# Kernel tuning notes

Measured on AMD Instinct MI355X. Metric: run time of the kernel, lower is better.

The kernel has to match this reference:

```python
import jax, jax.numpy as jnp
import numpy as np

DIM = 256
HEADS = 8
DHEAD = 32          # dim // 8
WIN = 128           # attn_window
NBLOCKS = 4
FF_INNER = int(DIM * 4 * 2 / 3)  # 682
SCALE = DHEAD ** -0.5


def layernorm(x, g, b):
    mu = jnp.mean(x, axis=-1, keepdims=True)
    var = jnp.mean((x - mu) ** 2, axis=-1, keepdims=True)
    return (x - mu) * jax.lax.rsqrt(var + 1e-5) * g + b


def look_around(x):
    # x: (b, h, nw, w, d) -> (b, h, nw, 3w, d); prev/current/next window, zero-padded ends
    nw = x.shape[2]
    p = jnp.pad(x, ((0, 0), (0, 0), (1, 1), (0, 0), (0, 0)))
    return jnp.concatenate([p[:, :, i:i + nw] for i in range(3)], axis=3)


def key_mask(mask):
    # mask: (b, n) bool -> (b, nw, 3w) validity of look-around keys
    b, n = mask.shape
    nw = n // WIN
    mb = mask.reshape(b, nw, WIN)
    p = jnp.pad(mb, ((0, 0), (1, 1), (0, 0)), constant_values=False)
    return jnp.concatenate([p[:, i:i + nw] for i in range(3)], axis=-1)


def local_mha(x, kmask, ln_g, ln_b, qkv_w, out_w):
    b, n, _ = x.shape
    nw = n // WIN
    xn = layernorm(x, ln_g, ln_b)
    qkv = jnp.einsum('bnd,ed->bne', xn, qkv_w)           # (b, n, 3*h*dh)
    qkv = qkv.reshape(b, nw, WIN, 3, HEADS, DHEAD)
    q, k, v = [jnp.transpose(qkv[:, :, :, i], (0, 3, 1, 2, 4)) for i in range(3)]  # (b,h,nw,w,dh)
    kk = look_around(k)                                   # (b,h,nw,3w,dh)
    vv = look_around(v)
    sim = jnp.einsum('bhnid,bhnjd->bhnij', q, kk) * SCALE  # (b,h,nw,w,3w)
    neg = -jnp.finfo(sim.dtype).max
    sim = jnp.where(kmask[:, None, :, None, :], sim, neg)
    attn = jax.nn.softmax(sim, axis=-1)
    out = jnp.einsum('bhnij,bhnjd->bhnid', attn, vv)      # (b,h,nw,w,dh)
    out = jnp.transpose(out, (0, 2, 3, 1, 4)).reshape(b, n, HEADS * DHEAD)
    return jnp.einsum('bne,de->bnd', out, out_w)


def geglu_ff(x, ln_g, ln_b, w1, w2):
    xn = layernorm(x, ln_g, ln_b)
    h = jnp.einsum('bnd,ed->bne', xn, w1)                 # (b, n, 2*FF_INNER)
    a, g = jnp.split(h, 2, axis=-1)
    y = a * jax.nn.gelu(g, approximate=False)             # exact GELU like torch
    return jnp.einsum('bne,de->bnd', y, w2)


def setup_inputs() -> dict:
    key = jax.random.key(0)
    ks = jax.random.split(key, 8)
    B, N = 8, 4096
    s = 0.02
    return {
        'x': jax.random.normal(ks[0], (B, N, DIM), dtype=jnp.float32),
        'mask': jnp.ones((B, N), dtype=bool),
        'ln1_g': jnp.ones((NBLOCKS, DIM), jnp.float32),
        'ln1_b': jnp.zeros((NBLOCKS, DIM), jnp.float32),
        'qkv_w': jax.random.normal(ks[1], (NBLOCKS, 3 * HEADS * DHEAD, DIM), jnp.float32) * s,
        'out_w': jax.random.normal(ks[2], (NBLOCKS, DIM, HEADS * DHEAD), jnp.float32) * s,
        'ln2_g': jnp.ones((NBLOCKS, DIM), jnp.float32),
        'ln2_b': jnp.zeros((NBLOCKS, DIM), jnp.float32),
        'ff_w1': jax.random.normal(ks[3], (NBLOCKS, 2 * FF_INNER, DIM), jnp.float32) * s,
        'ff_w2': jax.random.normal(ks[4], (NBLOCKS, DIM, FF_INNER), jnp.float32) * s,
    }


def reference(x, mask, ln1_g, ln1_b, qkv_w, out_w, ln2_g, ln2_b, ff_w1, ff_w2):
    kmask = key_mask(mask)
    for i in range(NBLOCKS):
        x = local_mha(x, kmask, ln1_g[i], ln1_b[i], qkv_w[i], out_w[i]) + x
        x = geglu_ff(x, ln2_g[i], ln2_b[i], ff_w1[i], ff_w2[i]) + x
    return x
```

## Files before the change

kernel.cpp:

```cpp
#include <hip/hip_runtime.h>


#define DIM 256
#define DHEAD 32
#define NWIN 32
#define SEQ 4096
#define TOKENS 32768
#define FFP 704
#define ATT_SCALE_LOG2E 0.25501818642228136f

typedef __attribute__((ext_vector_type(4))) float f32x4;
typedef __attribute__((ext_vector_type(4))) short s16x4;
typedef __attribute__((ext_vector_type(8))) short s16x8;
typedef __attribute__((ext_vector_type(4))) _Float16 f16x4;
typedef __attribute__((ext_vector_type(8))) _Float16 f16x8;

__device__ __forceinline__ short f2bf(float f) {
  unsigned int u = __float_as_uint(f);
  u += 0x7fffu + ((u >> 16) & 1u);
  return (short)(u >> 16);
}

__device__ __forceinline__ float fast_exp2(float x) {
#if __has_builtin(__builtin_amdgcn_exp2f)
  return __builtin_amdgcn_exp2f(x);
#else
  return __expf(x * 0.6931471805599453f);
#endif
}

__device__ __forceinline__ float gelu_exact(float g) {
  return 0.5f * g * (1.0f + erff(g * 0.70710678118654752440f));
}

__device__ __forceinline__ void gl_lds16(const short* g, short* l) {
  __builtin_amdgcn_global_load_lds(
      (const __attribute__((address_space(1))) void*)g,
      (__attribute__((address_space(3))) void*)l, 16, 0, 0);
}

__global__ void __launch_bounds__(256)
ln_kernel(const float* __restrict__ x, const float* __restrict__ gw,
          const float* __restrict__ bw, short* __restrict__ xn) {
  const int row = blockIdx.x * 4 + (threadIdx.x >> 6);
  const int lane = threadIdx.x & 63;
  const f32x4 v = *(const f32x4*)(x + (size_t)row * DIM + lane * 4);
  float s = v[0] + v[1] + v[2] + v[3];
  float s2 = v[0]*v[0] + v[1]*v[1] + v[2]*v[2] + v[3]*v[3];
#pragma unroll
  for (int off = 32; off > 0; off >>= 1) {
    s  += __shfl_xor(s, off, 64);
    s2 += __shfl_xor(s2, off, 64);
  }
  const float mu = s * (1.0f / DIM);
  const float var = s2 * (1.0f / DIM) - mu * mu;
  const float rstd = rsqrtf(var + 1e-5f);
  const f32x4 gv = *(const f32x4*)(gw + lane * 4);
  const f32x4 bv = *(const f32x4*)(bw + lane * 4);
  s16x4 o;
#pragma unroll
  for (int j = 0; j < 4; ++j) o[j] = f2bf((v[j] - mu) * rstd * gv[j] + bv[j]);
  *(s16x4*)(xn + (size_t)row * DIM + lane * 4) = o;
}

template<int K, bool RES>
__global__ void __launch_bounds__(256)
gemm128(const short* __restrict__ A, const short* __restrict__ W,
        void* __restrict__ outp, int Nout) {
  __shared__ short As[128 * 32];
  __shared__ short Bs[128 * 32];
  const int tid = threadIdx.x;
  const int lane = tid & 63;
  const int w = tid >> 6;
  const int ln16 = lane & 15;
  const int quad = lane >> 4;
  const int m_blk = blockIdx.x * 128;
  const int n_blk = blockIdx.y * 128;

  const int srow = lane >> 2;
  const int scol = (lane & 3) * 8;
  const short* Ag0 = A + (size_t)(m_blk + w * 32 + srow) * K + scol;
  const short* Ag1 = Ag0 + (size_t)16 * K;
  const short* Wg0 = W + (size_t)(n_blk + w * 32 + srow) * K + scol;
  const short* Wg1 = Wg0 + (size_t)16 * K;
  short* Al0 = As + w * 1024;
  short* Al1 = As + w * 1024 + 512;
  short* Bl0 = Bs + w * 1024;
  short* Bl1 = Bs + w * 1024 + 512;

  const int m0w = (w & 1) * 64;
  const int n0w = (w >> 1) * 64;
  f32x4 acc[4][4] = {};

  for (int kb = 0; kb < K; kb += 32) {
    gl_lds16(Ag0 + kb, Al0);
    gl_lds16(Ag1 + kb, Al1);
    gl_lds16(Wg0 + kb, Bl0);
    gl_lds16(Wg1 + kb, Bl1);
    __syncthreads();
    s16x8 af[4], bf[4];
#pragma unroll
    for (int mt = 0; mt < 4; ++mt)
      af[mt] = *(const s16x8*)(As + (m0w + mt * 16 + ln16) * 32 + quad * 8);
#pragma unroll
    for (int nt = 0; nt < 4; ++nt)
      bf[nt] = *(const s16x8*)(Bs + (n0w + nt * 16 + ln16) * 32 + quad * 8);
#pragma unroll
    for (int mt = 0; mt < 4; ++mt)
#pragma unroll
      for (int nt = 0; nt < 4; ++nt)
        acc[mt][nt] = __builtin_amdgcn_mfma_f32_16x16x32_bf16(af[mt], bf[nt], acc[mt][nt], 0, 0, 0);
    __syncthreads();
  }

  if (RES) {
    float* o = (float*)outp;
#pragma unroll
    for (int mt = 0; mt < 4; ++mt)
#pragma unroll
      for (int nt = 0; nt < 4; ++nt)
#pragma unroll
        for (int r = 0; r < 4; ++r) {
          const size_t idx = (size_t)(m_blk + m0w + mt * 16 + quad * 4 + r) * Nout
                             + n_blk + n0w + nt * 16 + ln16;
          o[idx] += acc[mt][nt][r];
        }
  } else {
    short* o = (short*)outp;
#pragma unroll
    for (int mt = 0; mt < 4; ++mt)
#pragma unroll
      for (int nt = 0; nt < 4; ++nt)
#pragma unroll
        for (int r = 0; r < 4; ++r)
          o[(size_t)(m_blk + m0w + mt * 16 + quad * 4 + r) * Nout
            + n_blk + n0w + nt * 16 + ln16] = f2bf(acc[mt][nt][r]);
  }
}

__global__ void __launch_bounds__(256)
gemm_qkv(const short* __restrict__ A, const short* __restrict__ W,
         short* __restrict__ qh, short* __restrict__ kh, _Float16* __restrict__ vp) {
  __shared__ short As[128 * 32];
  __shared__ short Bs[128 * 32];
  const int tid = threadIdx.x;
  const int lane = tid & 63;
  const int w = tid >> 6;
  const int ln16 = lane & 15;
  const int quad = lane >> 4;
  const int m_blk = blockIdx.x * 128;
  const int n_blk = blockIdx.y * 128;

  const int srow = lane >> 2;
  const int scol = (lane & 3) * 8;
  const short* Ag0 = A + (size_t)(m_blk + w * 32 + srow) * DIM + scol;
  const short* Ag1 = Ag0 + (size_t)16 * DIM;
  const short* Wg0 = W + (size_t)(n_blk + w * 32 + srow) * DIM + scol;
  const short* Wg1 = Wg0 + (size_t)16 * DIM;
  short* Al0 = As + w * 1024;
  short* Al1 = As + w * 1024 + 512;
  short* Bl0 = Bs + w * 1024;
  short* Bl1 = Bs + w * 1024 + 512;

  const int m0w = (w & 1) * 64;
  const int n0w = (w >> 1) * 64;
  f32x4 acc[4][4] = {};

  for (int kb = 0; kb < DIM; kb += 32) {
    gl_lds16(Ag0 + kb, Al0);
    gl_lds16(Ag1 + kb, Al1);
    gl_lds16(Wg0 + kb, Bl0);
    gl_lds16(Wg1 + kb, Bl1);
    __syncthreads();
    s16x8 af[4], bf[4];
#pragma unroll
    for (int mt = 0; mt < 4; ++mt)
      af[mt] = *(const s16x8*)(As + (m0w + mt * 16 + ln16) * 32 + quad * 8);
#pragma unroll
    for (int nt = 0; nt < 4; ++nt)
      bf[nt] = *(const s16x8*)(Bs + (n0w + nt * 16 + ln16) * 32 + quad * 8);
#pragma unroll
    for (int mt = 0; mt < 4; ++mt)
#pragma unroll
      for (int nt = 0; nt < 4; ++nt)
        acc[mt][nt] = __builtin_amdgcn_mfma_f32_16x16x32_bf16(af[mt], bf[nt], acc[mt][nt], 0, 0, 0);
    __syncthreads();
  }

#pragma unroll
  for (int mt = 0; mt < 4; ++mt) {
    const int m = m_blk + m0w + mt * 16 + quad * 4;
    const int bb = m >> 12;
    const int n = m & 4095;
#pragma unroll
    for (int nt = 0; nt < 4; ++nt) {
      const int f = n_blk + n0w + nt * 16;
      if (f < 512) {
        const int ff = f & 255;
        short* dst = (f < 256 ? qh : kh)
                     + ((size_t)(bb * 8 + (ff >> 5)) * SEQ + n) * 32 + (ff & 16) + ln16;
#pragma unroll
        for (int r = 0; r < 4; ++r) dst[r * 32] = f2bf(acc[mt][nt][r]);
      } else {
        const int ff = f - 512;
        const int h = ff >> 5;
        const int d = (ff & 16) + ln16;
        const int within = n & 31;
        const int pos = (n & ~31) + ((within & 12) << 1) + ((within >> 4) << 2);
        f16x4 o;
#pragma unroll
        for (int r = 0; r < 4; ++r) o[r] = (_Float16)acc[mt][nt][r];
        *(f16x4*)(vp + ((size_t)(bb * 8 + h) * 32 + d) * SEQ + pos) = o;
      }
    }
  }
}

__global__ void __launch_bounds__(256)
gemm_geglu128(const short* __restrict__ A, const short* __restrict__ W,
              short* __restrict__ y) {
  __shared__ short As[128 * 32];
  __shared__ short Bs[2 * 64 * 32];
  const int tid = threadIdx.x;
  const int lane = tid & 63;
  const int w = tid >> 6;
  const int ln16 = lane & 15;
  const int quad = lane >> 4;
  const int m_blk = blockIdx.x * 128;
  const int n0 = blockIdx.y * 64;

  const int srow = lane >> 2;
  const int scol = (lane & 3) * 8;
  const short* Ag0 = A + (size_t)(m_blk + w * 32 + srow) * DIM + scol;
  const short* Ag1 = Ag0 + (size_t)16 * DIM;
  const int gid0 = w * 2;
  const int half0 = gid0 >> 2, r16_0 = gid0 & 3;
  const int gid1 = w * 2 + 1;
  const int half1 = gid1 >> 2, r16_1 = gid1 & 3;
  const short* Wg0 = W + (size_t)(half0 * FFP + n0 + r16_0 * 16 + srow) * DIM + scol;
  const short* Wg1 = W + (size_t)(half1 * FFP + n0 + r16_1 * 16 + srow) * DIM + scol;
  short* Al0 = As + w * 1024;
  short* Al1 = As + w * 1024 + 512;
  short* Bl0 = Bs + half0 * 2048 + r16_0 * 512;
  short* Bl1 = Bs + half1 * 2048 + r16_1 * 512;

  const int m0w = (w & 1) * 64;
  const int n0w = (w >> 1) * 32;
  f32x4 acc[2][4][2] = {};

  for (int kb = 0; kb < DIM; kb += 32) {
    gl_lds16(Ag0 + kb, Al0);
    gl_lds16(Ag1 + kb, Al1);
    gl_lds16(Wg0 + kb, Bl0);
    gl_lds16(Wg1 + kb, Bl1);
    __syncthreads();
    s16x8 af[4], ba[2], bg[2];
#pragma unroll
    for (int mt = 0; mt < 4; ++mt)
      af[mt] = *(const s16x8*)(As + (m0w + mt * 16 + ln16) * 32 + quad * 8);
#pragma unroll
    for (int nt = 0; nt < 2; ++nt) {
      ba[nt] = *(const s16x8*)(Bs + (n0w + nt * 16 + ln16) * 32 + quad * 8);
      bg[nt] = *(const s16x8*)(Bs + 2048 + (n0w + nt * 16 + ln16) * 32 + quad * 8);
    }
#pragma unroll
    for (int mt = 0; mt < 4; ++mt)
#pragma unroll
      for (int nt = 0; nt < 2; ++nt) {
        acc[0][mt][nt] = __builtin_amdgcn_mfma_f32_16x16x32_bf16(af[mt], ba[nt], acc[0][mt][nt], 0, 0, 0);
        acc[1][mt][nt] = __builtin_amdgcn_mfma_f32_16x16x32_bf16(af[mt], bg[nt], acc[1][mt][nt], 0, 0, 0);
      }
    __syncthreads();
  }

#pragma unroll
  for (int mt = 0; mt < 4; ++mt)
#pragma unroll
    for (int nt = 0; nt < 2; ++nt)
#pragma unroll
      for (int r = 0; r < 4; ++r)
        y[(size_t)(m_blk + m0w + mt * 16 + quad * 4 + r) * FFP
          + n0 + n0w + nt * 16 + ln16] =
            f2bf(acc[0][mt][nt][r] * gelu_exact(acc[1][mt][nt][r]));
}

__global__ void __launch_bounds__(256)
attn_kernel(const short* __restrict__ qh, const short* __restrict__ kh,
            const _Float16* __restrict__ vp, short* __restrict__ out) {
  const int blk = blockIdx.x;
  const int lane = threadIdx.x & 63;
  const int wid = threadIdx.x >> 6;
  const int ln16 = lane & 15;
  const int quad = lane >> 4;

  const int w = (blk & 15) * 2 + (wid >> 1);
  const int h = (blk >> 4) & 7;
  const int b = blk >> 7;
  const int plane = b * 8 + h;
  const int tok0 = w * 128 + (wid & 1) * 64;
  const int ktok = w * 128 - 128;
  const int c0 = (w == 0) ? 4 : 0;
  const int c1 = (w == NWIN - 1) ? 8 : 12;

  const short* qp = qh + ((size_t)plane * SEQ + tok0) * 32;
  s16x8 qf[4];
#pragma unroll
  for (int qi = 0; qi < 4; ++qi)
    qf[qi] = *(const s16x8*)(qp + (qi * 16 + ln16) * 32 + quad * 8);

  const short* kp = kh + ((size_t)plane * SEQ + ktok) * 32;
  const _Float16* vb = vp + ((size_t)plane * 32 + ln16) * SEQ + ktok;

  float lsum[4] = {0.f, 0.f, 0.f, 0.f};
  f32x4 ot[4][2] = {};

  s16x8 kc0 = *(const s16x8*)(kp + (c0 * 32 + ln16) * 32 + quad * 8);
  s16x8 kc1 = *(const s16x8*)(kp + (c0 * 32 + 16 + ln16) * 32 + quad * 8);
  f16x8 vc0 = *(const f16x8*)(vb + c0 * 32 + quad * 8);
  f16x8 vc1 = *(const f16x8*)(vb + (size_t)16 * SEQ + c0 * 32 + quad * 8);

  for (int c = c0; c < c1; ++c) {
    const int cn = (c + 1 < c1) ? c + 1 : c;
    s16x8 kn0 = *(const s16x8*)(kp + (cn * 32 + ln16) * 32 + quad * 8);
    s16x8 kn1 = *(const s16x8*)(kp + (cn * 32 + 16 + ln16) * 32 + quad * 8);
    f16x8 vn0 = *(const f16x8*)(vb + cn * 32 + quad * 8);
    f16x8 vn1 = *(const f16x8*)(vb + (size_t)16 * SEQ + cn * 32 + quad * 8);

    const f16x4 v00 = __builtin_shufflevector(vc0, vc0, 0, 1, 2, 3);
    const f16x4 v10 = __builtin_shufflevector(vc0, vc0, 4, 5, 6, 7);
    const f16x4 v01 = __builtin_shufflevector(vc1, vc1, 0, 1, 2, 3);
    const f16x4 v11 = __builtin_shufflevector(vc1, vc1, 4, 5, 6, 7);

#pragma unroll
    for (int qi = 0; qi < 4; ++qi) {
      const f32x4 z = {0.f, 0.f, 0.f, 0.f};
      f32x4 st0 = __builtin_amdgcn_mfma_f32_16x16x32_bf16(kc0, qf[qi], z, 0, 0, 0);
      f32x4 st1 = __builtin_amdgcn_mfma_f32_16x16x32_bf16(kc1, qf[qi], z, 0, 0, 0);
      float p[8];
#pragma unroll
      for (int r = 0; r < 4; ++r) {
        p[r]     = fast_exp2(st0[r] * ATT_SCALE_LOG2E);
        p[4 + r] = fast_exp2(st1[r] * ATT_SCALE_LOG2E);
      }
      lsum[qi] += ((p[0] + p[1]) + (p[2] + p[3])) + ((p[4] + p[5]) + (p[6] + p[7]));
      f16x4 pa, pb;
#pragma unroll
      for (int r = 0; r < 4; ++r) { pa[r] = (_Float16)p[r]; pb[r] = (_Float16)p[4 + r]; }
      ot[qi][0] = __builtin_amdgcn_mfma_f32_16x16x16f16(pa, v00, ot[qi][0], 0, 0, 0);
      ot[qi][1] = __builtin_amdgcn_mfma_f32_16x16x16f16(pa, v01, ot[qi][1], 0, 0, 0);
      ot[qi][0] = __builtin_amdgcn_mfma_f32_16x16x16f16(pb, v10, ot[qi][0], 0, 0, 0);
      ot[qi][1] = __builtin_amdgcn_mfma_f32_16x16x16f16(pb, v11, ot[qi][1], 0, 0, 0);
    }
    kc0 = kn0; kc1 = kn1; vc0 = vn0; vc1 = vn1;
  }

#pragma unroll
  for (int qi = 0; qi < 4; ++qi) {
    float l = lsum[qi];
    l += __shfl_xor(l, 16, 64);
    l += __shfl_xor(l, 32, 64);
    const float inv = 1.0f / l;
#pragma unroll
    for (int dt = 0; dt < 2; ++dt)
#pragma unroll
      for (int r = 0; r < 4; ++r)
        out[(size_t)(b * SEQ + tok0 + qi * 16 + quad * 4 + r) * DIM
            + h * DHEAD + dt * 16 + ln16] = f2bf(ot[qi][dt][r] * inv);
  }
}

__global__ void cvt_copy(const float* __restrict__ s, short* __restrict__ d, int n) {
  const int i = blockIdx.x * 256 + threadIdx.x;
  if (i < n) d[i] = f2bf(s[i]);
}

__global__ void cvt_ff1(const float* __restrict__ s, short* __restrict__ d) {
  const int i = blockIdx.x * 256 + threadIdx.x;
  const int c = i & 255;
  const int rl = i >> 8;
  const int l = rl / 1408;
  const int r = rl - l * 1408;
  const int half = r / FFP;
  const int rr = r - half * FFP;
  const float v = (rr < 682) ? s[((size_t)(l * 1364 + half * 682 + rr)) * 256 + c] : 0.0f;
  d[i] = f2bf(v);
}

__global__ void cvt_ff2(const float* __restrict__ s, short* __restrict__ d) {
  const int i = blockIdx.x * 256 + threadIdx.x;
  const int c = i % FFP;
  const int t = i / FFP;
  const float v = (c < 682) ? s[(size_t)t * 682 + c] : 0.0f;
  d[i] = f2bf(v);
}

extern "C" void kernel_launch(void* const* d_in, const int* in_sizes, int n_in,
                              void* d_out, int out_size, void* d_ws, size_t ws_size,
                              hipStream_t stream) {
  const float* x0    = (const float*)d_in[0];
  const float* ln1_g = (const float*)d_in[2];
  const float* ln1_b = (const float*)d_in[3];
  const float* qkv_w = (const float*)d_in[4];
  const float* out_w = (const float*)d_in[5];
  const float* ln2_g = (const float*)d_in[6];
  const float* ln2_b = (const float*)d_in[7];
  const float* ff_w1 = (const float*)d_in[8];
  const float* ff_w2 = (const float*)d_in[9];
  float* x = (float*)d_out;

  char* ws = (char*)d_ws;
  short* wqkv = (short*)(ws);
  short* wout = (short*)(ws + 1572864);
  short* wff1 = (short*)(ws + 2097152);
  short* wff2 = (short*)(ws + 4980736);
  short* xn   = (short*)(ws + 6422528);
  short*    qhb = (short*)(ws + 23199744);
  short*    khb = (short*)(ws + 23199744 + 16777216);
  _Float16* vpb = (_Float16*)(ws + 23199744 + 33554432);
  short*    yb  = (short*)(ws + 23199744);

  hipMemcpyAsync(x, x0, (size_t)TOKENS * DIM * sizeof(float),
                 hipMemcpyDeviceToDevice, stream);
  cvt_copy<<<3072, 256, 0, stream>>>(qkv_w, wqkv, 786432);
  cvt_copy<<<1024, 256, 0, stream>>>(out_w, wout, 262144);
  cvt_ff1<<<5632, 256, 0, stream>>>(ff_w1, wff1);
  cvt_ff2<<<2816, 256, 0, stream>>>(ff_w2, wff2);

  for (int l = 0; l < 4; ++l) {
    ln_kernel<<<8192, 256, 0, stream>>>(x, ln1_g + l * DIM, ln1_b + l * DIM, xn);
    gemm_qkv<<<dim3(256, 6), 256, 0, stream>>>(
        xn, wqkv + (size_t)l * 768 * DIM, qhb, khb, vpb);
    attn_kernel<<<1024, 256, 0, stream>>>(qhb, khb, vpb, xn);
    gemm128<256, true><<<dim3(256, 2), 256, 0, stream>>>(
        xn, wout + (size_t)l * DIM * DIM, x, DIM);
    ln_kernel<<<8192, 256, 0, stream>>>(x, ln2_g + l * DIM, ln2_b + l * DIM, xn);
    gemm_geglu128<<<dim3(256, 11), 256, 0, stream>>>(
        xn, wff1 + (size_t)l * 2 * FFP * DIM, yb);
    gemm128<FFP, true><<<dim3(256, 2), 256, 0, stream>>>(
        yb, wff2 + (size_t)l * DIM * FFP, x, DIM);
  }
}
```

Measured before the change: 818.6 us.

## Fuse LayerNorm into residual GEMM epilogue and merge setup kernels

The residual-add GEMMs now use 512-thread blocks that each cover a full 256-wide output row tile. Their epilogue computes per-row LayerNorm statistics through shuffles and an LDS reduction, then writes the normalized bf16 activations for the next stage. This removes the standalone LayerNorm passes over the fp32 residual stream. The initial copy is fused with the first LayerNorm, and the four weight-conversion kernels are merged into one launch. In exchange there are half as many GEMM blocks, each doing more epilogue work and an extra barrier.

```diff
diff --git a/kernel.cpp b/kernel.cpp
--- a/kernel.cpp
+++ b/kernel.cpp
@@ -40,11 +40,12 @@
 }
 
 __global__ void __launch_bounds__(256)
-ln_kernel(const float* __restrict__ x, const float* __restrict__ gw,
-          const float* __restrict__ bw, short* __restrict__ xn) {
+copy_ln(const float* __restrict__ x0, const float* __restrict__ gw,
+        const float* __restrict__ bw, float* __restrict__ x, short* __restrict__ xn) {
   const int row = blockIdx.x * 4 + (threadIdx.x >> 6);
   const int lane = threadIdx.x & 63;
-  const f32x4 v = *(const f32x4*)(x + (size_t)row * DIM + lane * 4);
+  const f32x4 v = *(const f32x4*)(x0 + (size_t)row * DIM + lane * 4);
+  *(f32x4*)(x + (size_t)row * DIM + lane * 4) = v;
   float s = v[0] + v[1] + v[2] + v[3];
   float s2 = v[0]*v[0] + v[1]*v[1] + v[2]*v[2] + v[3]*v[3];
 #pragma unroll
@@ -63,40 +64,43 @@
   *(s16x4*)(xn + (size_t)row * DIM + lane * 4) = o;
 }
 
-template<int K, bool RES>
-__global__ void __launch_bounds__(256)
-gemm128(const short* __restrict__ A, const short* __restrict__ W,
-        void* __restrict__ outp, int Nout) {
+template<int K, bool DO_LN>
+__global__ void __launch_bounds__(512)
+gemm_res_ln(const short* __restrict__ A, const short* __restrict__ W,
+            float* __restrict__ x, const float* __restrict__ lng,
+            const float* __restrict__ lnb, short* __restrict__ xn) {
   __shared__ short As[128 * 32];
-  __shared__ short Bs[128 * 32];
+  __shared__ short Bs[256 * 32];
   const int tid = threadIdx.x;
   const int lane = tid & 63;
   const int w = tid >> 6;
   const int ln16 = lane & 15;
   const int quad = lane >> 4;
   const int m_blk = blockIdx.x * 128;
-  const int n_blk = blockIdx.y * 128;
-
+  const int m0w = (w & 1) * 64;
+  const int n0w = (w >> 1) * 64;
   const int srow = lane >> 2;
   const int scol = (lane & 3) * 8;
-  const short* Ag0 = A + (size_t)(m_blk + w * 32 + srow) * K + scol;
-  const short* Ag1 = Ag0 + (size_t)16 * K;
-  const short* Wg0 = W + (size_t)(n_blk + w * 32 + srow) * K + scol;
-  const short* Wg1 = Wg0 + (size_t)16 * K;
-  short* Al0 = As + w * 1024;
-  short* Al1 = As + w * 1024 + 512;
-  short* Bl0 = Bs + w * 1024;
-  short* Bl1 = Bs + w * 1024 + 512;
-
-  const int m0w = (w & 1) * 64;
-  const int n0w = (w >> 1) * 64;
+
+  const short* sg[3];
+  short* dg[3];
+#pragma unroll
+  for (int i = 0; i < 3; ++i) {
+    const int grp = w + i * 8;
+    if (grp < 8) {
+      sg[i] = A + (size_t)(m_blk + grp * 16 + srow) * K + scol;
+      dg[i] = As + grp * 512;
+    } else {
+      const int gb = grp - 8;
+      sg[i] = W + (size_t)(gb * 16 + srow) * K + scol;
+      dg[i] = Bs + gb * 512;
+    }
+  }
+
   f32x4 acc[4][4] = {};
-
   for (int kb = 0; kb < K; kb += 32) {
-    gl_lds16(Ag0 + kb, Al0);
-    gl_lds16(Ag1 + kb, Al1);
-    gl_lds16(Wg0 + kb, Bl0);
-    gl_lds16(Wg1 + kb, Bl1);
+#pragma unroll
+    for (int i = 0; i < 3; ++i) gl_lds16(sg[i] + kb, dg[i]);
     __syncthreads();
     s16x8 af[4], bf[4];
 #pragma unroll
@@ -113,28 +117,66 @@
     __syncthreads();
   }
 
-  if (RES) {
-    float* o = (float*)outp;
-#pragma unroll
-    for (int mt = 0; mt < 4; ++mt)
-#pragma unroll
-      for (int nt = 0; nt < 4; ++nt)
-#pragma unroll
-        for (int r = 0; r < 4; ++r) {
-          const size_t idx = (size_t)(m_blk + m0w + mt * 16 + quad * 4 + r) * Nout
-                             + n_blk + n0w + nt * 16 + ln16;
-          o[idx] += acc[mt][nt][r];
+#pragma unroll
+  for (int mt = 0; mt < 4; ++mt)
+#pragma unroll
+    for (int nt = 0; nt < 4; ++nt)
+#pragma unroll
+      for (int r = 0; r < 4; ++r) {
+        const size_t idx = (size_t)(m_blk + m0w + mt * 16 + quad * 4 + r) * DIM
+                           + n0w + nt * 16 + ln16;
+        const float v = x[idx] + acc[mt][nt][r];
+        acc[mt][nt][r] = v;
+        x[idx] = v;
+      }
+
+  if (DO_LN) {
+    float2* red = (float2*)As;
+#pragma unroll
+    for (int mt = 0; mt < 4; ++mt)
+#pragma unroll
+      for (int r = 0; r < 4; ++r) {
+        float s = 0.f, s2 = 0.f;
+#pragma unroll
+        for (int nt = 0; nt < 4; ++nt) {
+          const float v = acc[mt][nt][r];
+          s += v; s2 += v * v;
         }
-  } else {
-    short* o = (short*)outp;
-#pragma unroll
-    for (int mt = 0; mt < 4; ++mt)
-#pragma unroll
-      for (int nt = 0; nt < 4; ++nt)
-#pragma unroll
-        for (int r = 0; r < 4; ++r)
-          o[(size_t)(m_blk + m0w + mt * 16 + quad * 4 + r) * Nout
-            + n_blk + n0w + nt * 16 + ln16] = f2bf(acc[mt][nt][r]);
+#pragma unroll
+        for (int off = 1; off < 16; off <<= 1) {
+          s  += __shfl_xor(s, off, 64);
+          s2 += __shfl_xor(s2, off, 64);
+        }
+        if (ln16 == 0)
+          red[(m0w + mt * 16 + quad * 4 + r) * 4 + (w >> 1)] = float2{s, s2};
+      }
+    __syncthreads();
+
+    float gv[4], bv[4];
+#pragma unroll
+    for (int nt = 0; nt < 4; ++nt) {
+      gv[nt] = lng[n0w + nt * 16 + ln16];
+      bv[nt] = lnb[n0w + nt * 16 + ln16];
+    }
+#pragma unroll
+    for (int mt = 0; mt < 4; ++mt)
+#pragma unroll
+      for (int r = 0; r < 4; ++r) {
+        const int row = m0w + mt * 16 + quad * 4 + r;
+        const float2 t0 = red[row * 4 + 0];
+        const float2 t1 = red[row * 4 + 1];
+        const float2 t2 = red[row * 4 + 2];
+        const float2 t3 = red[row * 4 + 3];
+        const float s  = (t0.x + t1.x) + (t2.x + t3.x);
+        const float s2 = (t0.y + t1.y) + (t2.y + t3.y);
+        const float mu = s * (1.0f / DIM);
+        const float var = s2 * (1.0f / DIM) - mu * mu;
+        const float rstd = rsqrtf(var + 1e-5f);
+#pragma unroll
+        for (int nt = 0; nt < 4; ++nt)
+          xn[(size_t)(m_blk + row) * DIM + n0w + nt * 16 + ln16] =
+              f2bf((acc[mt][nt][r] - mu) * rstd * gv[nt] + bv[nt]);
+      }
   }
 }
 
@@ -369,29 +411,33 @@
   }
 }
 
-__global__ void cvt_copy(const float* __restrict__ s, short* __restrict__ d, int n) {
-  const int i = blockIdx.x * 256 + threadIdx.x;
-  if (i < n) d[i] = f2bf(s[i]);
-}
-
-__global__ void cvt_ff1(const float* __restrict__ s, short* __restrict__ d) {
-  const int i = blockIdx.x * 256 + threadIdx.x;
-  const int c = i & 255;
-  const int rl = i >> 8;
-  const int l = rl / 1408;
-  const int r = rl - l * 1408;
-  const int half = r / FFP;
-  const int rr = r - half * FFP;
-  const float v = (rr < 682) ? s[((size_t)(l * 1364 + half * 682 + rr)) * 256 + c] : 0.0f;
-  d[i] = f2bf(v);
-}
-
-__global__ void cvt_ff2(const float* __restrict__ s, short* __restrict__ d) {
-  const int i = blockIdx.x * 256 + threadIdx.x;
-  const int c = i % FFP;
-  const int t = i / FFP;
-  const float v = (c < 682) ? s[(size_t)t * 682 + c] : 0.0f;
-  d[i] = f2bf(v);
+__global__ void cvt_all(const float* __restrict__ qkv_w, const float* __restrict__ out_w,
+                        const float* __restrict__ ff_w1, const float* __restrict__ ff_w2,
+                        short* __restrict__ wqkv, short* __restrict__ wout,
+                        short* __restrict__ wff1, short* __restrict__ wff2) {
+  int i = blockIdx.x * 256 + threadIdx.x;
+  if (i < 786432) { wqkv[i] = f2bf(qkv_w[i]); return; }
+  i -= 786432;
+  if (i < 262144) { wout[i] = f2bf(out_w[i]); return; }
+  i -= 262144;
+  if (i < 1441792) {
+    const int c = i & 255;
+    const int rl = i >> 8;
+    const int l = rl / 1408;
+    const int r = rl - l * 1408;
+    const int half = r / FFP;
+    const int rr = r - half * FFP;
+    const float v = (rr < 682) ? ff_w1[((size_t)(l * 1364 + half * 682 + rr)) * 256 + c] : 0.0f;
+    wff1[i] = f2bf(v);
+    return;
+  }
+  i -= 1441792;
+  if (i < 720896) {
+    const int c = i % FFP;
+    const int t = i / FFP;
+    const float v = (c < 682) ? ff_w2[(size_t)t * 682 + c] : 0.0f;
+    wff2[i] = f2bf(v);
+  }
 }
 
 extern "C" void kernel_launch(void* const* d_in, const int* in_sizes, int n_in,
@@ -419,24 +465,24 @@
   _Float16* vpb = (_Float16*)(ws + 23199744 + 33554432);
   short*    yb  = (short*)(ws + 23199744);
 
-  hipMemcpyAsync(x, x0, (size_t)TOKENS * DIM * sizeof(float),
-                 hipMemcpyDeviceToDevice, stream);
-  cvt_copy<<<3072, 256, 0, stream>>>(qkv_w, wqkv, 786432);
-  cvt_copy<<<1024, 256, 0, stream>>>(out_w, wout, 262144);
-  cvt_ff1<<<5632, 256, 0, stream>>>(ff_w1, wff1);
-  cvt_ff2<<<2816, 256, 0, stream>>>(ff_w2, wff2);
+  copy_ln<<<8192, 256, 0, stream>>>(x0, ln1_g, ln1_b, x, xn);
+  cvt_all<<<12544, 256, 0, stream>>>(qkv_w, out_w, ff_w1, ff_w2, wqkv, wout, wff1, wff2);
 
   for (int l = 0; l < 4; ++l) {
-    ln_kernel<<<8192, 256, 0, stream>>>(x, ln1_g + l * DIM, ln1_b + l * DIM, xn);
     gemm_qkv<<<dim3(256, 6), 256, 0, stream>>>(
         xn, wqkv + (size_t)l * 768 * DIM, qhb, khb, vpb);
     attn_kernel<<<1024, 256, 0, stream>>>(qhb, khb, vpb, xn);
-    gemm128<256, true><<<dim3(256, 2), 256, 0, stream>>>(
-        xn, wout + (size_t)l * DIM * DIM, x, DIM);
-    ln_kernel<<<8192, 256, 0, stream>>>(x, ln2_g + l * DIM, ln2_b + l * DIM, xn);
+    gemm_res_ln<256, true><<<256, 512, 0, stream>>>(
+        xn, wout + (size_t)l * DIM * DIM, x,
+        ln2_g + l * DIM, ln2_b + l * DIM, xn);
     gemm_geglu128<<<dim3(256, 11), 256, 0, stream>>>(
         xn, wff1 + (size_t)l * 2 * FFP * DIM, yb);
-    gemm128<FFP, true><<<dim3(256, 2), 256, 0, stream>>>(
-        yb, wff2 + (size_t)l * DIM * FFP, x, DIM);
-  }
-}
+    if (l < 3)
+      gemm_res_ln<FFP, true><<<256, 512, 0, stream>>>(
+          yb, wff2 + (size_t)l * DIM * FFP, x,
+          ln1_g + (l + 1) * DIM, ln1_b + (l + 1) * DIM, xn);
+    else
+      gemm_res_ln<FFP, false><<<256, 512, 0, stream>>>(
+          yb, wff2 + (size_t)l * DIM * FFP, x, nullptr, nullptr, nullptr);
+  }
+}
```

Result: faster. 778.3 us (-4.9%).
